# Kernel optimization log

Measured on AMD Instinct MI355X. Metric: run time of the kernel, lower is better.

## Reference

```python
import jax, jax.numpy as jnp
import numpy as np

WS = (7, 7)  # window size
NUM_HEADS = 16


def _relative_position_index(ws):
    # Deterministic int index table, computed exactly as in the torch module.
    coords = np.stack(np.meshgrid(np.arange(ws[0]), np.arange(ws[1]), indexing='ij'))  # [2,Wh,Ww]
    coords = coords.reshape(2, -1)                       # [2, N]
    rel = coords[:, :, None] - coords[:, None, :]        # [2, N, N]
    rel = rel.transpose(1, 2, 0)                         # [N, N, 2]
    rel = rel + np.array([ws[0] - 1, ws[1] - 1])
    rel[:, :, 0] *= 2 * ws[1] - 1
    return jnp.asarray(rel.sum(-1), dtype=jnp.int32)     # [N, N]


def setup_inputs() -> dict:
    key = jax.random.key(0)
    ks = jax.random.split(key, 5)
    B_, N, C = 2048, WS[0] * WS[1], 512
    nw = 64
    return {
        'x': jax.random.normal(ks[0], (B_, N, C), dtype=jnp.float32),
        'mask': jax.random.normal(ks[1], (nw, N, N), dtype=jnp.float32),
        'qkv_w': jax.random.normal(ks[2], (3 * C, C), dtype=jnp.float32) * 0.02,
        'qkv_b': jax.random.normal(ks[3], (3 * C,), dtype=jnp.float32) * 0.02,
        'rpb_table': jax.random.normal(ks[4], ((2 * WS[0] - 1) * (2 * WS[1] - 1), NUM_HEADS), dtype=jnp.float32) * 0.02,
    }


def reference(x, mask, qkv_w, qkv_b, rpb_table):
    B_, N, C = x.shape
    H = NUM_HEADS
    hd = C // H
    scale = hd ** -0.5

    # qkv projection: [B_, N, 3, H, hd] -> q, k, v each [B_, H, N, hd]
    qkv = (jnp.einsum('bnc,oc->bno', x, qkv_w) + qkv_b)
    qkv = qkv.reshape(B_, N, 3, H, hd).transpose(2, 0, 3, 1, 4)
    q, k, v = qkv[0], qkv[1], qkv[2]

    attn = jnp.einsum('bhnd,bhmd->bhnm', q * scale, k)  # [B_, H, N, N]

    rel_idx = _relative_position_index(WS)                       # [N, N]
    bias = rpb_table[rel_idx.reshape(-1)].reshape(N, N, H)       # gather
    attn = attn + bias.transpose(2, 0, 1)[None]                  # [1, H, N, N]

    nw = mask.shape[0]
    attn = attn.reshape(B_ // nw, nw, H, N, N) + mask[None, :, None]
    attn = attn.reshape(B_, H, N, N)
    attn = jax.nn.softmax(attn, axis=-1)

    out = jnp.einsum('bhnm,bhmd->bhnd', attn, v)
    out = out.transpose(0, 2, 1, 3).reshape(B_, N, C)
    # NOTE: source assigns `X = self.proj(x)` but returns `x`, so the
    # output projection is dead code; we faithfully return pre-proj output.
    return out
```

## Files before the change

kernel.cpp:

```cpp
#include <hip/hip_runtime.h>
#include <cstdint>
#include <cstddef>

typedef __bf16 bf16x8 __attribute__((ext_vector_type(8)));
typedef float f32x4 __attribute__((ext_vector_type(4)));
typedef unsigned short u16x8 __attribute__((ext_vector_type(8)));
typedef unsigned short u16x4 __attribute__((ext_vector_type(4)));
typedef unsigned int u32x2 __attribute__((ext_vector_type(2)));

#define VT_LD 56
#define BSTRIDE 52
#define BSZ 2548
#define PLD 80

__device__ __forceinline__ unsigned short f2bf(float f) {
  unsigned int u = __builtin_bit_cast(unsigned int, f);
  u += 0x7FFFu + ((u >> 16) & 1u);
  return (unsigned short)(u >> 16);
}
__device__ __forceinline__ float bf2f(unsigned short h) {
  unsigned int u = (unsigned int)h << 16;
  return __builtin_bit_cast(float, u);
}

__device__ __forceinline__ void gload_lds16(const void* g, void* l) {
  __builtin_amdgcn_global_load_lds((const __attribute__((address_space(1))) void*)g,
                                   (__attribute__((address_space(3))) void*)l, 16, 0, 0);
}

__global__ void conv_f2b_k(const float* __restrict__ src, unsigned short* __restrict__ dst, long n8) {
  long i = (long)blockIdx.x * blockDim.x + threadIdx.x;
  long stride = (long)gridDim.x * blockDim.x;
  for (; i < n8; i += stride) {
    float4 a = *(const float4*)(src + i * 8);
    float4 b = *(const float4*)(src + i * 8 + 4);
    u16x8 p;
    p[0]=f2bf(a.x); p[1]=f2bf(a.y); p[2]=f2bf(a.z); p[3]=f2bf(a.w);
    p[4]=f2bf(b.x); p[5]=f2bf(b.y); p[6]=f2bf(b.z); p[7]=f2bf(b.w);
    *(u16x8*)(dst + i * 8) = p;
  }
}

__global__ void build_bias_k(const float* __restrict__ rpb, unsigned short* __restrict__ biasT) {
  int idx = blockIdx.x * 256 + threadIdx.x;
  if (idx >= 16 * BSZ) return;
  int h = idx / BSZ;
  int rem = idx - h * BSZ;
  int i = rem / BSTRIDE, j = rem - (rem / BSTRIDE) * BSTRIDE;
  unsigned short v = 0;
  if (j < 49) {
    int r1 = i / 7, c1 = i - r1 * 7;
    int r2 = j / 7, c2 = j - r2 * 7;
    int ri = (r1 - r2 + 6) * 13 + (c1 - c2 + 6);
    v = f2bf(rpb[ri * 16 + h]);
  }
  biasT[idx] = v;
}

#define GEMM_SETUP(N0)                                                         \
  int t = threadIdx.x;                                                         \
  int lane = t & 63, wv = t >> 6;                                              \
  int g = lane >> 4, q = lane & 15;                                            \
  int wrow = wv >> 1, wcol = wv & 1;                                           \
  f32x4 acc[4][4] = {};                                                        \
  int schunk = (t & 3) ^ ((t >> 3) & 3);                                       \
  const unsigned short* ag0 = xb + (m0 + (t >> 2)) * 512 + schunk * 8;         \
  const unsigned short* ag1 = ag0 + 64 * 512;                                  \
  const unsigned short* bg0 = wb + (size_t)((N0) + (t >> 2)) * 512 + schunk * 8; \
  const unsigned short* bg1 = bg0 + 64 * 512;                                  \
  unsigned short* alA  = Ab + wv * 512;                                        \
  unsigned short* alA2 = Ab + 2048 + wv * 512;                                 \
  unsigned short* blB  = Bb + wv * 512;                                        \
  unsigned short* blB2 = Bb + 2048 + wv * 512;                                 \
  int roff = (8 * g) ^ (((q >> 1) & 3) << 3);                                  \
  const unsigned short* arb = Ab + (wrow * 64 + q) * 32 + roff;                \
  const unsigned short* brb = Bb + (wcol * 64 + q) * 32 + roff;

#define STAGE(KT, BOFF) do {                    \
    int kof = (KT) * 32;                        \
    gload_lds16(ag0 + kof, alA  + (BOFF));      \
    gload_lds16(ag1 + kof, alA2 + (BOFF));      \
    gload_lds16(bg0 + kof, blB  + (BOFF));      \
    gload_lds16(bg1 + kof, blB2 + (BOFF));      \
  } while (0)

#define COMPUTE(BOFF, SWAPPED) do {                                            \
    bf16x8 af[4], bfr[4];                                                      \
    _Pragma("unroll")                                                          \
    for (int i2 = 0; i2 < 4; ++i2) af[i2]  = *(const bf16x8*)(arb + (BOFF) + i2 * 512); \
    _Pragma("unroll")                                                          \
    for (int j2 = 0; j2 < 4; ++j2) bfr[j2] = *(const bf16x8*)(brb + (BOFF) + j2 * 512); \
    _Pragma("unroll")                                                          \
    for (int i2 = 0; i2 < 4; ++i2)                                             \
      _Pragma("unroll")                                                        \
      for (int j2 = 0; j2 < 4; ++j2)                                           \
        acc[i2][j2] = (SWAPPED)                                                \
          ? __builtin_amdgcn_mfma_f32_16x16x32_bf16(bfr[j2], af[i2], acc[i2][j2], 0, 0, 0) \
          : __builtin_amdgcn_mfma_f32_16x16x32_bf16(af[i2], bfr[j2], acc[i2][j2], 0, 0, 0); \
  } while (0)

#define KLOOP(SWAPPED)                                                 \
  STAGE(0, 0);                                                         \
  STAGE(1, 4096);                                                      \
  asm volatile("s_waitcnt vmcnt(4)" ::: "memory");                     \
  __builtin_amdgcn_s_barrier();                                        \
  _Pragma("unroll")                                                    \
  for (int kt = 0; kt < 16; ++kt) {                                    \
    if (kt + 2 < 16) STAGE(kt + 2, ((kt + 2) % 3) * 4096);             \
    COMPUTE((kt % 3) * 4096, SWAPPED);                                 \
    if (kt < 15) {                                                     \
      if (kt + 2 < 16) asm volatile("s_waitcnt vmcnt(4)" ::: "memory"); \
      else             asm volatile("s_waitcnt vmcnt(0)" ::: "memory"); \
      __builtin_amdgcn_s_barrier();                                    \
    }                                                                  \
  }

__global__ __launch_bounds__(256, 3) void qkv_gemm_k(
    const unsigned short* __restrict__ xb, const float* __restrict__ qkv_b,
    const unsigned short* __restrict__ wb,
    unsigned short* __restrict__ qs, unsigned short* __restrict__ kk,
    unsigned short* __restrict__ vt)
{
  __shared__ __align__(16) unsigned short smem[24576];
  unsigned short* Ab = smem;
  unsigned short* Bb = smem + 12288;

  int bid = blockIdx.x;
  int sw = (bid & 7) * 1176 + (bid >> 3);
  int mt = sw / 12, nt = sw - mt * 12;
  long m0 = (long)mt * 128;
  int  n0 = nt * 128;
  int  s  = n0 >> 9;

  GEMM_SETUP(n0)

  if (s < 2) {
    KLOOP(1)
    unsigned short* dst = (s == 0) ? qs : kk;
    float sc = (s == 0) ? 0.17677669529663687f : 1.0f;
    float4 bi[4];
    int hj[4], dj[4];
    #pragma unroll
    for (int j2 = 0; j2 < 4; ++j2) {
      int n = n0 + wcol * 64 + j2 * 16 + 4 * g;
      bi[j2] = *(const float4*)(qkv_b + n);
      hj[j2] = (n >> 5) & 15;
      dj[j2] = n & 31;
    }
    #pragma unroll
    for (int i2 = 0; i2 < 4; ++i2) {
      unsigned int m = (unsigned int)m0 + wrow * 64 + i2 * 16 + q;
      unsigned int b = m / 49;
      unsigned int i = m - b * 49;
      size_t base = ((size_t)(b * 16) * 49 + i) * 32;
      #pragma unroll
      for (int j2 = 0; j2 < 4; ++j2) {
        f32x4 a = acc[i2][j2];
        unsigned int lo = (unsigned int)f2bf((a[0] + bi[j2].x) * sc) | ((unsigned int)f2bf((a[1] + bi[j2].y) * sc) << 16);
        unsigned int hi = (unsigned int)f2bf((a[2] + bi[j2].z) * sc) | ((unsigned int)f2bf((a[3] + bi[j2].w) * sc) << 16);
        u32x2 wv2 = {lo, hi};
        *(u32x2*)(dst + base + (size_t)hj[j2] * (49 * 32) + dj[j2]) = wv2;
      }
    }
  } else {
    KLOOP(0)
    #pragma unroll
    for (int j2 = 0; j2 < 4; ++j2) {
      int n  = n0 + wcol * 64 + j2 * 16 + q;
      float bias = qkv_b[n];
      int d = n & 31;
      int h = (n >> 5) & 15;
      #pragma unroll
      for (int i2 = 0; i2 < 4; ++i2) {
        unsigned int gm0 = (unsigned int)m0 + wrow * 64 + i2 * 16 + 4 * g;
        unsigned int b0 = gm0 / 49;
        unsigned int i0 = gm0 - b0 * 49;
        unsigned short hv[4];
        #pragma unroll
        for (int r = 0; r < 4; ++r) hv[r] = f2bf(acc[i2][j2][r] + bias);
        if (i0 <= 45) {
          unsigned short* base = vt + ((size_t)(b0 * 16 + h) * 32 + d) * VT_LD;
          if ((i0 & 1) == 0) {
            *(unsigned int*)(base + i0)     = (unsigned int)hv[0] | ((unsigned int)hv[1] << 16);
            *(unsigned int*)(base + i0 + 2) = (unsigned int)hv[2] | ((unsigned int)hv[3] << 16);
          } else {
            base[i0] = hv[0];
            *(unsigned int*)(base + i0 + 1) = (unsigned int)hv[1] | ((unsigned int)hv[2] << 16);
            base[i0 + 3] = hv[3];
          }
        } else {
          #pragma unroll
          for (int r = 0; r < 4; ++r) {
            unsigned int gm = gm0 + r;
            unsigned int b = gm / 49;
            unsigned int i = gm - b * 49;
            vt[((size_t)(b * 16 + h) * 32 + d) * VT_LD + i] = hv[r];
          }
        }
      }
    }
  }
}

__global__ __launch_bounds__(256, 2) void win_attn_k(
    const unsigned short* __restrict__ qs, const unsigned short* __restrict__ kk,
    const unsigned short* __restrict__ vt, const unsigned short* __restrict__ biasT,
    const float* __restrict__ mask, float* __restrict__ out)
{
  __shared__ float mlds[BSZ];
  __shared__ unsigned short plds[4][64 * PLD];

  int b = blockIdx.x;
  int t = threadIdx.x;
  int lane = t & 63, wv = t >> 6;
  int g = lane >> 4, q = lane & 15;

  const float* msrc = mask + (size_t)(b & 63) * 2401;
  for (int idx = t; idx < BSZ; idx += 256) {
    int i = idx / BSTRIDE, j = idx - (idx / BSTRIDE) * BSTRIDE;
    mlds[idx] = (j < 49) ? msrc[i * 49 + j] : 0.0f;
  }
  __syncthreads();

  unsigned short* pl = plds[wv];
  const float NINF = -__builtin_inff();

  int rc[4];
  rc[0] = q; rc[1] = 16 + q; rc[2] = 32 + q; rc[3] = 48;

  int h0 = wv * 4;
  const unsigned short* qh = qs + (size_t)(b * 16 + h0) * (49 * 32);
  const unsigned short* kh = kk + (size_t)(b * 16 + h0) * (49 * 32);
  bf16x8 ak[4], bq[4];
  #pragma unroll
  for (int jt = 0; jt < 4; ++jt) ak[jt] = *(const bf16x8*)(kh + rc[jt] * 32 + 8 * g);
  #pragma unroll
  for (int it = 0; it < 4; ++it) bq[it] = *(const bf16x8*)(qh + rc[it] * 32 + 8 * g);

  #pragma unroll
  for (int hh = 0; hh < 4; ++hh) {
    int h = wv * 4 + hh;
    const unsigned short* vh  = vt + (size_t)(b * 16 + h) * (32 * VT_LD);
    const unsigned short* bh2 = biasT + h * BSZ;

    f32x4 zero = {0.f, 0.f, 0.f, 0.f};
    f32x4 st[4][4];
    __builtin_amdgcn_s_setprio(1);
    #pragma unroll
    for (int it = 0; it < 4; ++it)
      #pragma unroll
      for (int jt = 0; jt < 4; ++jt)
        st[it][jt] = __builtin_amdgcn_mfma_f32_16x16x32_bf16(ak[jt], bq[it], zero, 0, 0, 0);
    __builtin_amdgcn_s_setprio(0);

    bf16x8 akn[4], bqn[4];
    if (hh < 3) {
      const unsigned short* qh2 = qh + 49 * 32;
      const unsigned short* kh2 = kh + 49 * 32;
      #pragma unroll
      for (int jt = 0; jt < 4; ++jt) akn[jt] = *(const bf16x8*)(kh2 + rc[jt] * 32 + 8 * g);
      #pragma unroll
      for (int it = 0; it < 4; ++it) bqn[it] = *(const bf16x8*)(qh2 + rc[it] * 32 + 8 * g);
      qh = qh2; kh = kh2;
    }
    bf16x8 bv[2][2];
    #pragma unroll
    for (int ktt = 0; ktt < 2; ++ktt)
      #pragma unroll
      for (int dt = 0; dt < 2; ++dt)
        bv[ktt][dt] = *(const bf16x8*)(vh + (dt * 16 + q) * VT_LD + ktt * 32 + 8 * g);

    #pragma unroll
    for (int it = 0; it < 4; ++it) {
      int i = it * 16 + q;
      int ic = i > 48 ? 48 : i;
      f32x4 pv4[4];
      f32x4 vm = {NINF, NINF, NINF, NINF};
      #pragma unroll
      for (int jt = 0; jt < 4; ++jt) {
        if (jt == 3 && g > 0) {
          pv4[3] = (f32x4){NINF, NINF, NINF, NINF};
        } else {
          u16x4 bu = *(const u16x4*)(bh2 + ic * BSTRIDE + jt * 16 + 4 * g);
          f32x4 m4 = *(const f32x4*)(mlds + ic * BSTRIDE + jt * 16 + 4 * g);
          f32x4 sv = st[it][jt];
          #pragma unroll
          for (int r = 0; r < 4; ++r) sv[r] += bf2f(bu[r]) + m4[r];
          if (jt == 3) {
            sv[1] = NINF; sv[2] = NINF; sv[3] = NINF;
          }
          pv4[jt] = sv;
          #pragma unroll
          for (int r = 0; r < 4; ++r) vm[r] = fmaxf(vm[r], sv[r]);
        }
      }
      float mx = fmaxf(fmaxf(vm[0], vm[1]), fmaxf(vm[2], vm[3]));
      mx = fmaxf(mx, __shfl_xor(mx, 16));
      mx = fmaxf(mx, __shfl_xor(mx, 32));
      f32x4 vs = zero;
      #pragma unroll
      for (int jt = 0; jt < 4; ++jt) {
        #pragma unroll
        for (int r = 0; r < 4; ++r) {
          float p = __expf(pv4[jt][r] - mx);
          pv4[jt][r] = p;
          vs[r] += p;
        }
      }
      float sm = (vs[0] + vs[1]) + (vs[2] + vs[3]);
      sm += __shfl_xor(sm, 16);
      sm += __shfl_xor(sm, 32);
      float rv = 1.0f / sm;
      #pragma unroll
      for (int jt = 0; jt < 4; ++jt) {
        unsigned int lo = (unsigned int)f2bf(pv4[jt][0] * rv) | ((unsigned int)f2bf(pv4[jt][1] * rv) << 16);
        unsigned int hi = (unsigned int)f2bf(pv4[jt][2] * rv) | ((unsigned int)f2bf(pv4[jt][3] * rv) << 16);
        u32x2 w = {lo, hi};
        *(u32x2*)(pl + i * PLD + jt * 16 + 4 * g) = w;
      }
    }

    f32x4 oacc[4][2] = {};
    #pragma unroll
    for (int ktt = 0; ktt < 2; ++ktt) {
      bf16x8 pa[4];
      #pragma unroll
      for (int it = 0; it < 4; ++it)
        pa[it] = *(const bf16x8*)(pl + (it * 16 + q) * PLD + ktt * 32 + 8 * g);
      __builtin_amdgcn_s_setprio(1);
      #pragma unroll
      for (int it = 0; it < 4; ++it)
        #pragma unroll
        for (int dt = 0; dt < 2; ++dt)
          oacc[it][dt] = __builtin_amdgcn_mfma_f32_16x16x32_bf16(bv[ktt][dt], pa[it], oacc[it][dt], 0, 0, 0);
      __builtin_amdgcn_s_setprio(0);
    }

    #pragma unroll
    for (int it = 0; it < 4; ++it) {
      int i = it * 16 + q;
      if (i < 49) {
        float* orow = out + (size_t)(b * 49 + i) * 512 + h * 32 + 4 * g;
        #pragma unroll
        for (int dt = 0; dt < 2; ++dt)
          *(f32x4*)(orow + dt * 16) = oacc[it][dt];
      }
    }

    if (hh < 3) {
      #pragma unroll
      for (int jt = 0; jt < 4; ++jt) ak[jt] = akn[jt];
      #pragma unroll
      for (int it = 0; it < 4; ++it) bq[it] = bqn[it];
    }
  }
}

extern "C" void kernel_launch(void* const* d_in, const int* in_sizes, int n_in,
                              void* d_out, int out_size, void* d_ws, size_t ws_size,
                              hipStream_t stream) {
  const float* x     = (const float*)d_in[0];
  const float* mask  = (const float*)d_in[1];
  const float* qkv_w = (const float*)d_in[2];
  const float* qkv_b = (const float*)d_in[3];
  const float* rpb   = (const float*)d_in[4];
  float* out = (float*)d_out;

  const size_t QS_OFF   = 0;
  const size_t KK_OFF   = 102760448;
  const size_t VT_OFF   = 205520896;
  const size_t BIAS_OFF = 322961408;
  const size_t WB_OFF   = 323042944;
  const size_t NEED     = 324615808;
  if (ws_size < NEED) return;

  char* ws = (char*)d_ws;
  unsigned short* qsb   = (unsigned short*)(ws + QS_OFF);
  unsigned short* kkb   = (unsigned short*)(ws + KK_OFF);
  unsigned short* vtb   = (unsigned short*)(ws + VT_OFF);
  unsigned short* biasT = (unsigned short*)(ws + BIAS_OFF);
  unsigned short* wb    = (unsigned short*)(ws + WB_OFF);

  unsigned short* xb = (unsigned short*)d_out;

  conv_f2b_k<<<2048, 256, 0, stream>>>(x, xb, 6422528);
  conv_f2b_k<<<512, 256, 0, stream>>>(qkv_w, wb, 98304);
  build_bias_k<<<160, 256, 0, stream>>>(rpb, biasT);
  qkv_gemm_k<<<9408, 256, 0, stream>>>(xb, qkv_b, wb, qsb, kkb, vtb);
  win_attn_k<<<2048, 256, 0, stream>>>(qsb, kkb, vtb, biasT, mask, out);
}
```

Before: 448.6 us.

## Replace 128x128 QKV GEMM with 256x256-tile 8-wave ping-pong pipelined kernel

The QKV projection GEMM moves from 128x128 tiles with 4 waves to 256x256 tiles with 8 waves and 64-wide K steps. Loads are double-buffered and issued in halves interleaved between four MFMA phases, with s_setprio raised around the MFMA blocks. Larger tiles increase operand reuse and cut the global traffic per FLOP. In exchange the kernel uses 128KB of LDS per block, more accumulator registers, and many more barriers, which lowers occupancy and leaves fewer blocks to spread across CUs.

```diff
diff --git a/kernel.cpp b/kernel.cpp
--- a/kernel.cpp
+++ b/kernel.cpp
@@ -57,127 +57,164 @@
   biasT[idx] = v;
 }
 
-#define GEMM_SETUP(N0)                                                         \
-  int t = threadIdx.x;                                                         \
-  int lane = t & 63, wv = t >> 6;                                              \
-  int g = lane >> 4, q = lane & 15;                                            \
-  int wrow = wv >> 1, wcol = wv & 1;                                           \
-  f32x4 acc[4][4] = {};                                                        \
-  int schunk = (t & 3) ^ ((t >> 3) & 3);                                       \
-  const unsigned short* ag0 = xb + (m0 + (t >> 2)) * 512 + schunk * 8;         \
-  const unsigned short* ag1 = ag0 + 64 * 512;                                  \
-  const unsigned short* bg0 = wb + (size_t)((N0) + (t >> 2)) * 512 + schunk * 8; \
-  const unsigned short* bg1 = bg0 + 64 * 512;                                  \
-  unsigned short* alA  = Ab + wv * 512;                                        \
-  unsigned short* alA2 = Ab + 2048 + wv * 512;                                 \
-  unsigned short* blB  = Bb + wv * 512;                                        \
-  unsigned short* blB2 = Bb + 2048 + wv * 512;                                 \
-  int roff = (8 * g) ^ (((q >> 1) & 3) << 3);                                  \
-  const unsigned short* arb = Ab + (wrow * 64 + q) * 32 + roff;                \
-  const unsigned short* brb = Bb + (wcol * 64 + q) * 32 + roff;
-
-#define STAGE(KT, BOFF) do {                    \
-    int kof = (KT) * 32;                        \
-    gload_lds16(ag0 + kof, alA  + (BOFF));      \
-    gload_lds16(ag1 + kof, alA2 + (BOFF));      \
-    gload_lds16(bg0 + kof, blB  + (BOFF));      \
-    gload_lds16(bg1 + kof, blB2 + (BOFF));      \
+
+#define STGA_H(KT, H) do {                                                                  \
+    gload_lds16(ags + (size_t)(H)*65536 + (KT)*64,      Ab + ((KT)&1)*16384 + (H)*4096 + wid*512);        \
+    gload_lds16(ags + (size_t)(H)*65536 + (KT)*64 + 32, Ab + ((KT)&1)*16384 + 8192 + (H)*4096 + wid*512); \
   } while (0)
-
-#define COMPUTE(BOFF, SWAPPED) do {                                            \
-    bf16x8 af[4], bfr[4];                                                      \
-    _Pragma("unroll")                                                          \
-    for (int i2 = 0; i2 < 4; ++i2) af[i2]  = *(const bf16x8*)(arb + (BOFF) + i2 * 512); \
-    _Pragma("unroll")                                                          \
-    for (int j2 = 0; j2 < 4; ++j2) bfr[j2] = *(const bf16x8*)(brb + (BOFF) + j2 * 512); \
-    _Pragma("unroll")                                                          \
-    for (int i2 = 0; i2 < 4; ++i2)                                             \
-      _Pragma("unroll")                                                        \
-      for (int j2 = 0; j2 < 4; ++j2)                                           \
-        acc[i2][j2] = (SWAPPED)                                                \
-          ? __builtin_amdgcn_mfma_f32_16x16x32_bf16(bfr[j2], af[i2], acc[i2][j2], 0, 0, 0) \
-          : __builtin_amdgcn_mfma_f32_16x16x32_bf16(af[i2], bfr[j2], acc[i2][j2], 0, 0, 0); \
+#define STGB_H(KT, H) do {                                                                  \
+    gload_lds16(bgs + (size_t)(H)*65536 + (KT)*64,      Bb + ((KT)&1)*16384 + (H)*4096 + wid*512);        \
+    gload_lds16(bgs + (size_t)(H)*65536 + (KT)*64 + 32, Bb + ((KT)&1)*16384 + 8192 + (H)*4096 + wid*512); \
   } while (0)
 
-#define KLOOP(SWAPPED)                                                 \
-  STAGE(0, 0);                                                         \
-  STAGE(1, 4096);                                                      \
-  asm volatile("s_waitcnt vmcnt(4)" ::: "memory");                     \
-  __builtin_amdgcn_s_barrier();                                        \
-  _Pragma("unroll")                                                    \
-  for (int kt = 0; kt < 16; ++kt) {                                    \
-    if (kt + 2 < 16) STAGE(kt + 2, ((kt + 2) % 3) * 4096);             \
-    COMPUTE((kt % 3) * 4096, SWAPPED);                                 \
-    if (kt < 15) {                                                     \
-      if (kt + 2 < 16) asm volatile("s_waitcnt vmcnt(4)" ::: "memory"); \
-      else             asm volatile("s_waitcnt vmcnt(0)" ::: "memory"); \
-      __builtin_amdgcn_s_barrier();                                    \
-    }                                                                  \
-  }
-
-__global__ __launch_bounds__(256, 3) void qkv_gemm_k(
+#define MPH(R2, C2, BF, SWAPPED) do {                                                       \
+    __builtin_amdgcn_s_setprio(1);                                                          \
+    _Pragma("unroll")                                                                       \
+    for (int rtl = 0; rtl < 4; ++rtl)                                                       \
+      _Pragma("unroll")                                                                     \
+      for (int ctl = 0; ctl < 2; ++ctl)                                                     \
+        _Pragma("unroll")                                                                   \
+        for (int ks2 = 0; ks2 < 2; ++ks2)                                                   \
+          acc[(R2)*4+rtl][(C2)*2+ctl] = (SWAPPED)                                           \
+            ? __builtin_amdgcn_mfma_f32_16x16x32_bf16(BF[ctl][ks2], af[rtl][ks2], acc[(R2)*4+rtl][(C2)*2+ctl], 0, 0, 0) \
+            : __builtin_amdgcn_mfma_f32_16x16x32_bf16(af[rtl][ks2], BF[ctl][ks2], acc[(R2)*4+rtl][(C2)*2+ctl], 0, 0, 0); \
+    __builtin_amdgcn_s_setprio(0);                                                          \
+  } while (0)
+
+#define TILE256(KT, BUF, SWAPPED) do {                                                      \
+                                     \
+    _Pragma("unroll")                                                                       \
+    for (int rtl = 0; rtl < 4; ++rtl) {                                                     \
+      af[rtl][0] = *(const bf16x8*)(arp + (BUF)*16384 + rtl*512);                           \
+      af[rtl][1] = *(const bf16x8*)(arp + (BUF)*16384 + 8192 + rtl*512);                    \
+    }                                                                                       \
+    _Pragma("unroll")                                                                       \
+    for (int ctl = 0; ctl < 2; ++ctl) {                                                     \
+      bf0[ctl][0] = *(const bf16x8*)(brp + (BUF)*16384 + ctl*512);                          \
+      bf0[ctl][1] = *(const bf16x8*)(brp + (BUF)*16384 + 8192 + ctl*512);                   \
+    }                                                                                       \
+    if ((KT) + 1 < 8) { STGA_H((KT)+1, 1); }                                                \
+    __builtin_amdgcn_s_barrier();                                                           \
+    MPH(0, 0, bf0, SWAPPED);                                                                \
+    __builtin_amdgcn_s_barrier();                                                           \
+                                                                 \
+    _Pragma("unroll")                                                                       \
+    for (int ctl = 0; ctl < 2; ++ctl) {                                                     \
+      bf1[ctl][0] = *(const bf16x8*)(brp + (BUF)*16384 + 1024 + ctl*512);                   \
+      bf1[ctl][1] = *(const bf16x8*)(brp + (BUF)*16384 + 8192 + 1024 + ctl*512);            \
+    }                                                                                       \
+    __builtin_amdgcn_s_barrier();                                                           \
+    MPH(0, 1, bf1, SWAPPED);                                                                \
+    __builtin_amdgcn_s_barrier();                                                           \
+                                               \
+    _Pragma("unroll")                                                                       \
+    for (int rtl = 0; rtl < 4; ++rtl) {                                                     \
+      af[rtl][0] = *(const bf16x8*)(arp + (BUF)*16384 + 2048 + rtl*512);                    \
+      af[rtl][1] = *(const bf16x8*)(arp + (BUF)*16384 + 8192 + 2048 + rtl*512);             \
+    }                                                                                       \
+    if ((KT) + 2 < 8) { STGB_H((KT)+2, 0); }                                                \
+    __builtin_amdgcn_s_barrier();                                                           \
+    MPH(1, 1, bf1, SWAPPED);                                                                \
+    __builtin_amdgcn_s_barrier();                                                           \
+                                 \
+    if ((KT) + 2 < 8) {                                                                     \
+      STGB_H((KT)+2, 1); STGA_H((KT)+2, 0);                                                 \
+      asm volatile("s_waitcnt vmcnt(6)" ::: "memory");                                      \
+    } else if ((KT) + 1 < 8) {                                                              \
+      asm volatile("s_waitcnt vmcnt(0)" ::: "memory");                                      \
+    }                                                                                       \
+    __builtin_amdgcn_s_barrier();                                                           \
+    MPH(1, 0, bf0, SWAPPED);                                                                \
+    __builtin_amdgcn_s_barrier();                                                           \
+  } while (0)
+
+__global__ __launch_bounds__(512, 2) void qkv_gemm256_k(
     const unsigned short* __restrict__ xb, const float* __restrict__ qkv_b,
     const unsigned short* __restrict__ wb,
     unsigned short* __restrict__ qs, unsigned short* __restrict__ kk,
     unsigned short* __restrict__ vt)
 {
-  __shared__ __align__(16) unsigned short smem[24576];
+  __shared__ __align__(16) unsigned short smem[65536];
   unsigned short* Ab = smem;
-  unsigned short* Bb = smem + 12288;
+  unsigned short* Bb = smem + 32768;
 
   int bid = blockIdx.x;
-  int sw = (bid & 7) * 1176 + (bid >> 3);
-  int mt = sw / 12, nt = sw - mt * 12;
-  long m0 = (long)mt * 128;
-  int  n0 = nt * 128;
+  int sw = (bid & 7) * 294 + (bid >> 3);
+  int mt = sw / 6, nt = sw - mt * 6;
+  long m0 = (long)mt * 256;
+  int  n0 = nt * 256;
   int  s  = n0 >> 9;
 
-  GEMM_SETUP(n0)
+  int t = threadIdx.x;
+  int lane = t & 63, wid = t >> 6;
+  int g = lane >> 4, q = lane & 15;
+  int wm = wid >> 2, wn = wid & 3;
+
+  f32x4 acc[8][4] = {};
+  bf16x8 af[4][2], bf0[2][2], bf1[2][2];
+
+  int schunk = (t & 3) ^ ((t >> 3) & 3);
+  const unsigned short* ags = xb + (m0 + (t >> 2)) * 512 + schunk * 8;
+  const unsigned short* bgs = wb + (size_t)(n0 + (t >> 2)) * 512 + schunk * 8;
+
+  int slot = (g ^ ((q >> 1) & 3)) * 8;
+  const unsigned short* arp = Ab + (wm * 128 + q) * 32 + slot;
+  const unsigned short* brp = Bb + (wn * 64 + q) * 32 + slot;
+
+  STGB_H(0, 0); STGB_H(0, 1); STGA_H(0, 0); STGA_H(0, 1);
+  STGB_H(1, 0); STGB_H(1, 1); STGA_H(1, 0);
+  asm volatile("s_waitcnt vmcnt(6)" ::: "memory");
+  __builtin_amdgcn_s_barrier();
 
   if (s < 2) {
-    KLOOP(1)
+    for (int kp = 0; kp < 4; ++kp) {
+      TILE256(2 * kp, 0, 1);
+      TILE256(2 * kp + 1, 1, 1);
+    }
     unsigned short* dst = (s == 0) ? qs : kk;
-    float sc = (s == 0) ? 0.17677669529663687f : 1.0f;
-    float4 bi[4];
-    int hj[4], dj[4];
-    #pragma unroll
-    for (int j2 = 0; j2 < 4; ++j2) {
-      int n = n0 + wcol * 64 + j2 * 16 + 4 * g;
-      bi[j2] = *(const float4*)(qkv_b + n);
-      hj[j2] = (n >> 5) & 15;
-      dj[j2] = n & 31;
-    }
-    #pragma unroll
-    for (int i2 = 0; i2 < 4; ++i2) {
-      unsigned int m = (unsigned int)m0 + wrow * 64 + i2 * 16 + q;
+    float sc2 = (s == 0) ? 0.17677669529663687f : 1.0f;
+    float4 bi[4]; int hj[4], dj[4];
+    #pragma unroll
+    for (int ct = 0; ct < 4; ++ct) {
+      int n4 = n0 + wn * 64 + ct * 16 + 4 * g;
+      bi[ct] = *(const float4*)(qkv_b + n4);
+      hj[ct] = (n4 >> 5) & 15;
+      dj[ct] = n4 & 31;
+    }
+    #pragma unroll
+    for (int rt = 0; rt < 8; ++rt) {
+      unsigned int m = (unsigned int)m0 + wm * 128 + rt * 16 + q;
       unsigned int b = m / 49;
       unsigned int i = m - b * 49;
       size_t base = ((size_t)(b * 16) * 49 + i) * 32;
       #pragma unroll
-      for (int j2 = 0; j2 < 4; ++j2) {
-        f32x4 a = acc[i2][j2];
-        unsigned int lo = (unsigned int)f2bf((a[0] + bi[j2].x) * sc) | ((unsigned int)f2bf((a[1] + bi[j2].y) * sc) << 16);
-        unsigned int hi = (unsigned int)f2bf((a[2] + bi[j2].z) * sc) | ((unsigned int)f2bf((a[3] + bi[j2].w) * sc) << 16);
+      for (int ct = 0; ct < 4; ++ct) {
+        f32x4 a = acc[rt][ct];
+        unsigned int lo = (unsigned int)f2bf((a[0] + bi[ct].x) * sc2) | ((unsigned int)f2bf((a[1] + bi[ct].y) * sc2) << 16);
+        unsigned int hi = (unsigned int)f2bf((a[2] + bi[ct].z) * sc2) | ((unsigned int)f2bf((a[3] + bi[ct].w) * sc2) << 16);
         u32x2 wv2 = {lo, hi};
-        *(u32x2*)(dst + base + (size_t)hj[j2] * (49 * 32) + dj[j2]) = wv2;
+        *(u32x2*)(dst + base + (size_t)hj[ct] * 1568 + dj[ct]) = wv2;
       }
     }
   } else {
-    KLOOP(0)
-    #pragma unroll
-    for (int j2 = 0; j2 < 4; ++j2) {
-      int n  = n0 + wcol * 64 + j2 * 16 + q;
+    for (int kp = 0; kp < 4; ++kp) {
+      TILE256(2 * kp, 0, 0);
+      TILE256(2 * kp + 1, 1, 0);
+    }
+    #pragma unroll
+    for (int ct = 0; ct < 4; ++ct) {
+      int n = n0 + wn * 64 + ct * 16 + q;
       float bias = qkv_b[n];
       int d = n & 31;
       int h = (n >> 5) & 15;
       #pragma unroll
-      for (int i2 = 0; i2 < 4; ++i2) {
-        unsigned int gm0 = (unsigned int)m0 + wrow * 64 + i2 * 16 + 4 * g;
+      for (int rt = 0; rt < 8; ++rt) {
+        unsigned int gm0 = (unsigned int)m0 + wm * 128 + rt * 16 + 4 * g;
         unsigned int b0 = gm0 / 49;
         unsigned int i0 = gm0 - b0 * 49;
         unsigned short hv[4];
         #pragma unroll
-        for (int r = 0; r < 4; ++r) hv[r] = f2bf(acc[i2][j2][r] + bias);
+        for (int r = 0; r < 4; ++r) hv[r] = f2bf(acc[rt][ct][r] + bias);
         if (i0 <= 45) {
           unsigned short* base = vt + ((size_t)(b0 * 16 + h) * 32 + d) * VT_LD;
           if ((i0 & 1) == 0) {
@@ -386,6 +423,6 @@
   conv_f2b_k<<<2048, 256, 0, stream>>>(x, xb, 6422528);
   conv_f2b_k<<<512, 256, 0, stream>>>(qkv_w, wb, 98304);
   build_bias_k<<<160, 256, 0, stream>>>(rpb, biasT);
-  qkv_gemm_k<<<9408, 256, 0, stream>>>(xb, qkv_b, wb, qsb, kkb, vtb);
+  qkv_gemm256_k<<<2352, 512, 0, stream>>>(xb, qkv_b, wb, qsb, kkb, vtb);
   win_attn_k<<<2048, 256, 0, stream>>>(qsb, kkb, vtb, biasT, mask, out);
 }
```

Result: faster. 429.9 us (-4.2%).
